# Optimization experiments

Hardware: AMD Instinct MI355X
Metric: run time of the kernel (lower is better)

Reference implementation:

```python
import jax, jax.numpy as jnp
import numpy as np

B, N, E = 32, 2000, 32000      # graphs, nodes/graph, edges/graph
V, D, R, K = 100000, 128, 39, 8  # vocab, emb_dim, n_relation, n_bases
EPS = 1e-5


def setup_inputs() -> dict:
    key = jax.random.key(0)
    ks = jax.random.split(key, 8)
    node_ids = jax.random.randint(ks[0], (B, N), 0, V)
    edge_index = jax.random.randint(ks[1], (B, 2, E), 0, N)
    edge_type = jax.random.randint(ks[2], (B, E), 0, R)
    embedding = jax.random.normal(ks[3], (V, D), jnp.float32) * D ** -0.5
    bases = jax.random.normal(ks[4], (K, D, D), jnp.float32) * D ** -0.5
    comp = jax.random.normal(ks[5], (R, K), jnp.float32) * K ** -0.5
    root = jax.random.normal(ks[6], (D, D), jnp.float32) * D ** -0.5
    bias = jnp.zeros((D,), jnp.float32)
    return dict(node_ids=node_ids, edge_index=edge_index, edge_type=edge_type,
                embedding=embedding, bases=bases, comp=comp, root=root, bias=bias)


def _graph_fwd(node_ids, edge_index, edge_type, embedding, bases, comp, root, bias):
    # RGCNConv with basis decomposition and per-relation MEAN aggregation (PyG default).
    x = embedding[node_ids]                       # [N, D] per-graph node features
    src, dst = edge_index[0], edge_index[1]       # j -> i, aggregate at dst
    x_src = x[src]                                # [E, D]
    # mean normalizer per (dst, relation) bucket
    comb = dst * R + edge_type                    # [E]
    cnt = jax.ops.segment_sum(jnp.ones((E,), jnp.float32), comb, num_segments=N * R)
    inv = jnp.where(cnt > 0, 1.0 / cnt, 0.0)[comb]  # [E]
    # W_r = sum_k comp[r,k] * bases[k]; fold comp coefficients + mean norm into edge weights
    w = comp[edge_type] * inv[:, None]            # [E, K]
    out = x @ root + bias                         # root/self connection
    for k in range(K):                            # small fixed loop over bases
        zk = jax.ops.segment_sum(w[:, k:k + 1] * x_src, dst, num_segments=N)  # [N, D]
        out = out + zk @ bases[k]
    g = out.sum(axis=0)                           # sum pool over nodes
    # torch.nn.functional.normalize(p=2, eps=1e-5)
    return g / jnp.maximum(jnp.linalg.norm(g), EPS)


def reference(node_ids, edge_index, edge_type, embedding, bases, comp, root, bias):
    f = jax.vmap(_graph_fwd, in_axes=(0, 0, 0, None, None, None, None, None))
    return f(node_ids, edge_index, edge_type, embedding, bases, comp, root, bias)  # [B, D]
```

## Files before the change

kernel.cpp:

```cpp
#include <hip/hip_runtime.h>
#include <math.h>

#define Bn 32
#define Nn 2000
#define En 32000
#define Vn 100000
#define Dn 128
#define Rn 39
#define Kn 8

#define SUBS 16
#define NPS (Nn / SUBS)
#define CH 64


__global__ __launch_bounds__(1024) void cnt_kernel(const int* __restrict__ edge_index,
                                                   const int* __restrict__ edge_type,
                                                   int* __restrict__ cnt) {
    int b = blockIdx.x, sub = blockIdx.y;
    int s0 = sub * NPS;
    __shared__ int loc[NPS * Rn];
    for (int i = threadIdx.x; i < NPS * Rn; i += 1024) loc[i] = 0;
    __syncthreads();
    const int* dstp = edge_index + (b * 2 + 1) * En;
    const int* etp  = edge_type + b * En;
    for (int e = threadIdx.x; e < En; e += 2048) {
        int du0 = dstp[e] - s0;
        int e1 = e + 1024;
        int du1 = (e1 < En) ? (dstp[e1] - s0) : -1;
        if ((unsigned)du0 < NPS) atomicAdd(&loc[du0 * Rn + etp[e]], 1);
        if ((unsigned)du1 < NPS) atomicAdd(&loc[du1 * Rn + etp[e1]], 1);
    }
    __syncthreads();
    int* g = cnt + ((size_t)b * Nn + s0) * Rn;
    for (int i = threadIdx.x; i < NPS * Rn; i += 1024) g[i] = loc[i];
}

__global__ __launch_bounds__(1024) void a_kernel(const int* __restrict__ edge_index,
                                                 const int* __restrict__ edge_type,
                                                 const int* __restrict__ cnt,
                                                 const float* __restrict__ comp,
                                                 float* __restrict__ a) {
    int b = blockIdx.x, sub = blockIdx.y;
    int s0 = sub * NPS;
    __shared__ float s[NPS * Rn];
    __shared__ float comp_l[Rn * Kn];
    for (int i = threadIdx.x; i < NPS * Rn; i += 1024) s[i] = 0.0f;
    if (threadIdx.x < Rn * Kn) comp_l[threadIdx.x] = comp[threadIdx.x];
    __syncthreads();
    const int* srcp = edge_index + (b * 2 + 0) * En;
    const int* dstp = edge_index + (b * 2 + 1) * En;
    const int* etp  = edge_type + b * En;
    const int* cb   = cnt + (size_t)b * Nn * Rn;
    for (int e = threadIdx.x; e < En; e += 2048) {
        int su0 = srcp[e] - s0;
        int e1 = e + 1024;
        int su1 = (e1 < En) ? (srcp[e1] - s0) : -1;
        if ((unsigned)su0 < NPS) {
            int t = etp[e];
            float inv = 1.0f / (float)cb[dstp[e] * Rn + t];
            atomicAdd(&s[su0 * Rn + t], inv);
        }
        if ((unsigned)su1 < NPS) {
            int t = etp[e1];
            float inv = 1.0f / (float)cb[dstp[e1] * Rn + t];
            atomicAdd(&s[su1 * Rn + t], inv);
        }
    }
    __syncthreads();
    float* g = a + ((size_t)b * Nn + s0) * Kn;
    for (int i = threadIdx.x; i < NPS * Kn; i += 1024) {
        int n = i >> 3, k = i & 7;
        float acc = 0.0f;
        const float* srow = &s[n * Rn];
        for (int t = 0; t < Rn; t++) acc += srow[t] * comp_l[t * Kn + k];
        g[i] = acc;
    }
}

__global__ __launch_bounds__(256) void gather_kernel(const int* __restrict__ node_ids,
                                                     const float* __restrict__ emb,
                                                     const float* __restrict__ a,
                                                     float* __restrict__ partial) {
    int b = blockIdx.x, c = blockIdx.y;
    int lane = threadIdx.x & 63, wv = threadIdx.x >> 6;
    float acc[18];
#pragma unroll
    for (int k = 0; k < 18; k++) acc[k] = 0.0f;
    const int* nb = node_ids + b * Nn;
    for (int n = c * 4 + wv; n < Nn; n += 2 * CH * 4) {
        int n2 = n + CH * 4;
        bool has2 = n2 < Nn;
        int nid  = nb[n];
        int nid2 = has2 ? nb[n2] : 0;
        float2 v  = ((const float2*)(emb + (size_t)nid  * Dn))[lane];
        float2 v2 = has2 ? ((const float2*)(emb + (size_t)nid2 * Dn))[lane]
                         : make_float2(0.f, 0.f);
        const float4* ar = (const float4*)(a + ((size_t)b * Nn + n) * Kn);
        float4 a0 = ar[0], a1 = ar[1];
        float w[9] = {a0.x, a0.y, a0.z, a0.w, a1.x, a1.y, a1.z, a1.w, 1.0f};
#pragma unroll
        for (int k = 0; k < 9; k++) { acc[2*k] += w[k] * v.x; acc[2*k+1] += w[k] * v.y; }
        if (has2) {
            const float4* ar2 = (const float4*)(a + ((size_t)b * Nn + n2) * Kn);
            float4 b0 = ar2[0], b1 = ar2[1];
            float w2[9] = {b0.x, b0.y, b0.z, b0.w, b1.x, b1.y, b1.z, b1.w, 1.0f};
#pragma unroll
            for (int k = 0; k < 9; k++) { acc[2*k] += w2[k] * v2.x; acc[2*k+1] += w2[k] * v2.y; }
        }
    }
    __shared__ float red[4 * 9 * Dn];
#pragma unroll
    for (int k = 0; k < 9; k++) {
        ((float2*)&red[(wv * 9 + k) * Dn])[lane] = make_float2(acc[2*k], acc[2*k+1]);
    }
    __syncthreads();
    float* g = partial + ((size_t)b * CH + c) * 9 * Dn;
    for (int i = threadIdx.x; i < 9 * Dn; i += 256)
        g[i] = red[i] + red[9 * Dn + i] + red[18 * Dn + i] + red[27 * Dn + i];
}

__global__ __launch_bounds__(256) void matvec_kernel(const float* __restrict__ partial,
                                                     const float* __restrict__ root,
                                                     const float* __restrict__ bases,
                                                     float* __restrict__ gmat) {
    int b = blockIdx.x, m = blockIdx.y;
    int d = threadIdx.x & (Dn - 1), h = threadIdx.x >> 7;
    __shared__ float ts[Dn];
    __shared__ float tsh[2][Dn];
    const float* p = partial + (size_t)b * CH * 9 * Dn + m * Dn + d;
    float sum = 0.0f;
    for (int c = h; c < CH; c += 2) sum += p[(size_t)c * 9 * Dn];
    tsh[h][d] = sum;
    __syncthreads();
    if (h == 0) ts[d] = tsh[0][d] + tsh[1][d];
    __syncthreads();
    const float* M = (m == 8) ? root : bases + (size_t)m * Dn * Dn;
    float g = 0.0f;
    for (int j = h * 64; j < h * 64 + 64; j++) g += ts[j] * M[j * Dn + d];
    __syncthreads();
    tsh[h][d] = g;
    __syncthreads();
    if (h == 0) gmat[((size_t)b * 9 + m) * Dn + d] = tsh[0][d] + tsh[1][d];
}

__global__ __launch_bounds__(128) void norm_kernel(const float* __restrict__ gmat,
                                                   const float* __restrict__ bias,
                                                   float* __restrict__ out) {
    int b = blockIdx.x, d = threadIdx.x;
    float g = (float)Nn * bias[d];
    const float* gb = gmat + (size_t)b * 9 * Dn + d;
#pragma unroll
    for (int m = 0; m < 9; m++) g += gb[m * Dn];
    float ss = g * g;
#pragma unroll
    for (int off = 32; off > 0; off >>= 1) ss += __shfl_down(ss, off, 64);
    __shared__ float s2[2];
    if ((threadIdx.x & 63) == 0) s2[threadIdx.x >> 6] = ss;
    __syncthreads();
    float nrm = sqrtf(s2[0] + s2[1]);
    out[b * Dn + d] = g / fmaxf(nrm, 1e-5f);
}

extern "C" void kernel_launch(void* const* d_in, const int* in_sizes, int n_in,
                              void* d_out, int out_size, void* d_ws, size_t ws_size,
                              hipStream_t stream) {
    const int*   node_ids   = (const int*)d_in[0];
    const int*   edge_index = (const int*)d_in[1];
    const int*   edge_type  = (const int*)d_in[2];
    const float* embedding  = (const float*)d_in[3];
    const float* bases      = (const float*)d_in[4];
    const float* comp       = (const float*)d_in[5];
    const float* root       = (const float*)d_in[6];
    const float* bias       = (const float*)d_in[7];
    float*       out        = (float*)d_out;

    int*   cnt     = (int*)d_ws;
    float* partial = (float*)d_ws;
    float* a       = (float*)((char*)d_ws + 9984000);
    float* gmat    = a;

    cnt_kernel   <<<dim3(Bn, SUBS), 1024, 0, stream>>>(edge_index, edge_type, cnt);
    a_kernel     <<<dim3(Bn, SUBS), 1024, 0, stream>>>(edge_index, edge_type, cnt, comp, a);
    gather_kernel<<<dim3(Bn, CH),   256,  0, stream>>>(node_ids, embedding, a, partial);
    matvec_kernel<<<dim3(Bn, 9),    256,  0, stream>>>(partial, root, bases, gmat);
    norm_kernel  <<<Bn, 128, 0, stream>>>(gmat, bias, out);
}
```

Measured before the change: 175.5 us.

## Precompute per-edge inverse counts, vectorize edge loads, rebalance sub-blocks and chunks

```diff
diff --git a/kernel.cpp b/kernel.cpp
--- a/kernel.cpp
+++ b/kernel.cpp
@@ -9,9 +9,10 @@
 #define Rn 39
 #define Kn 8
 
-#define SUBS 16
+#define SUBS 8
 #define NPS (Nn / SUBS)
-#define CH 64
+#define CH 128
+#define EQ (En / 4)
 
 
 __global__ __launch_bounds__(1024) void cnt_kernel(const int* __restrict__ edge_index,
@@ -22,23 +23,43 @@
     __shared__ int loc[NPS * Rn];
     for (int i = threadIdx.x; i < NPS * Rn; i += 1024) loc[i] = 0;
     __syncthreads();
-    const int* dstp = edge_index + (b * 2 + 1) * En;
-    const int* etp  = edge_type + b * En;
-    for (int e = threadIdx.x; e < En; e += 2048) {
-        int du0 = dstp[e] - s0;
-        int e1 = e + 1024;
-        int du1 = (e1 < En) ? (dstp[e1] - s0) : -1;
-        if ((unsigned)du0 < NPS) atomicAdd(&loc[du0 * Rn + etp[e]], 1);
-        if ((unsigned)du1 < NPS) atomicAdd(&loc[du1 * Rn + etp[e1]], 1);
+    const int4* dst4 = (const int4*)(edge_index + (b * 2 + 1) * En);
+    const int4* et4  = (const int4*)(edge_type + b * En);
+    for (int q = threadIdx.x; q < EQ; q += 1024) {
+        int4 d = dst4[q];
+        int4 t = et4[q];
+        int x;
+        x = d.x - s0; if ((unsigned)x < NPS) atomicAdd(&loc[x * Rn + t.x], 1);
+        x = d.y - s0; if ((unsigned)x < NPS) atomicAdd(&loc[x * Rn + t.y], 1);
+        x = d.z - s0; if ((unsigned)x < NPS) atomicAdd(&loc[x * Rn + t.z], 1);
+        x = d.w - s0; if ((unsigned)x < NPS) atomicAdd(&loc[x * Rn + t.w], 1);
     }
     __syncthreads();
     int* g = cnt + ((size_t)b * Nn + s0) * Rn;
     for (int i = threadIdx.x; i < NPS * Rn; i += 1024) g[i] = loc[i];
 }
 
+__global__ __launch_bounds__(256) void inv_kernel(const int* __restrict__ edge_index,
+                                                  const int* __restrict__ edge_type,
+                                                  const int* __restrict__ cnt,
+                                                  float* __restrict__ inv) {
+    int b = blockIdx.x;
+    int q = blockIdx.y * 256 + threadIdx.x;
+    if (q >= EQ) return;
+    int4 d = ((const int4*)(edge_index + (b * 2 + 1) * En))[q];
+    int4 t = ((const int4*)(edge_type + b * En))[q];
+    const int* cb = cnt + (size_t)b * Nn * Rn;
+    float4 r;
+    r.x = 1.0f / (float)cb[d.x * Rn + t.x];
+    r.y = 1.0f / (float)cb[d.y * Rn + t.y];
+    r.z = 1.0f / (float)cb[d.z * Rn + t.z];
+    r.w = 1.0f / (float)cb[d.w * Rn + t.w];
+    ((float4*)(inv + (size_t)b * En))[q] = r;
+}
+
 __global__ __launch_bounds__(1024) void a_kernel(const int* __restrict__ edge_index,
                                                  const int* __restrict__ edge_type,
-                                                 const int* __restrict__ cnt,
+                                                 const float* __restrict__ inv,
                                                  const float* __restrict__ comp,
                                                  float* __restrict__ a) {
     int b = blockIdx.x, sub = blockIdx.y;
@@ -48,24 +69,18 @@
     for (int i = threadIdx.x; i < NPS * Rn; i += 1024) s[i] = 0.0f;
     if (threadIdx.x < Rn * Kn) comp_l[threadIdx.x] = comp[threadIdx.x];
     __syncthreads();
-    const int* srcp = edge_index + (b * 2 + 0) * En;
-    const int* dstp = edge_index + (b * 2 + 1) * En;
-    const int* etp  = edge_type + b * En;
-    const int* cb   = cnt + (size_t)b * Nn * Rn;
-    for (int e = threadIdx.x; e < En; e += 2048) {
-        int su0 = srcp[e] - s0;
-        int e1 = e + 1024;
-        int su1 = (e1 < En) ? (srcp[e1] - s0) : -1;
-        if ((unsigned)su0 < NPS) {
-            int t = etp[e];
-            float inv = 1.0f / (float)cb[dstp[e] * Rn + t];
-            atomicAdd(&s[su0 * Rn + t], inv);
-        }
-        if ((unsigned)su1 < NPS) {
-            int t = etp[e1];
-            float inv = 1.0f / (float)cb[dstp[e1] * Rn + t];
-            atomicAdd(&s[su1 * Rn + t], inv);
-        }
+    const int4*   src4 = (const int4*)(edge_index + (b * 2 + 0) * En);
+    const int4*   et4  = (const int4*)(edge_type + b * En);
+    const float4* iv4  = (const float4*)(inv + (size_t)b * En);
+    for (int q = threadIdx.x; q < EQ; q += 1024) {
+        int4 sv = src4[q];
+        int4 tv = et4[q];
+        float4 iv = iv4[q];
+        int x;
+        x = sv.x - s0; if ((unsigned)x < NPS) atomicAdd(&s[x * Rn + tv.x], iv.x);
+        x = sv.y - s0; if ((unsigned)x < NPS) atomicAdd(&s[x * Rn + tv.y], iv.y);
+        x = sv.z - s0; if ((unsigned)x < NPS) atomicAdd(&s[x * Rn + tv.z], iv.z);
+        x = sv.w - s0; if ((unsigned)x < NPS) atomicAdd(&s[x * Rn + tv.w], iv.w);
     }
     __syncthreads();
     float* g = a + ((size_t)b * Nn + s0) * Kn;
@@ -175,13 +190,16 @@
     const float* bias       = (const float*)d_in[7];
     float*       out        = (float*)d_out;
 
-    int*   cnt     = (int*)d_ws;
-    float* partial = (float*)d_ws;
-    float* a       = (float*)((char*)d_ws + 9984000);
-    float* gmat    = a;
+    char* w = (char*)d_ws;
+    int*   cnt     = (int*)  (w + 0);
+    float* inv     = (float*)(w + 9984000);
+    float* a       = (float*)(w + 14080000);
+    float* partial = (float*)(w + 16128000);
+    float* gmat    = (float*)(w + 35004416);
 
     cnt_kernel   <<<dim3(Bn, SUBS), 1024, 0, stream>>>(edge_index, edge_type, cnt);
-    a_kernel     <<<dim3(Bn, SUBS), 1024, 0, stream>>>(edge_index, edge_type, cnt, comp, a);
+    inv_kernel   <<<dim3(Bn, (EQ + 255) / 256), 256, 0, stream>>>(edge_index, edge_type, cnt, inv);
+    a_kernel     <<<dim3(Bn, SUBS), 1024, 0, stream>>>(edge_index, edge_type, inv, comp, a);
     gather_kernel<<<dim3(Bn, CH),   256,  0, stream>>>(node_ids, embedding, a, partial);
     matvec_kernel<<<dim3(Bn, 9),    256,  0, stream>>>(partial, root, bases, gmat);
     norm_kernel  <<<Bn, 128, 0, stream>>>(gmat, bias, out);
```

New measurement: 166.7 us. -5.0%, faster.
